# Optimization experiments

Measured on AMD Instinct MI355X. Metric: run time of the kernel, lower is better.

Reference implementation:

```python
import jax, jax.numpy as jnp
import numpy as np

N_NODES = 100000
N_EDGES = 1600000
IN, HID, OUT = 64, 64, 32


def setup_inputs() -> dict:
    key = jax.random.key(0)
    ks = jax.random.split(key, 8)
    x = jax.random.normal(ks[0], (N_NODES, IN), dtype=jnp.float32)
    src = jax.random.randint(ks[1], (N_EDGES,), 0, N_NODES)
    dst = jax.random.randint(ks[2], (N_EDGES,), 0, N_NODES)
    s = 0.05
    return {
        "x": x,
        "src": src,
        "dst": dst,
        "W_self1": jax.random.normal(ks[3], (IN, HID), dtype=jnp.float32) * s,
        "W_neigh1": jax.random.normal(ks[4], (IN, HID), dtype=jnp.float32) * s,
        "b1": jnp.zeros((HID,), dtype=jnp.float32),
        "W_self2": jax.random.normal(ks[5], (HID, OUT), dtype=jnp.float32) * s,
        "W_neigh2": jax.random.normal(ks[6], (HID, OUT), dtype=jnp.float32) * s,
        "b2": jnp.zeros((OUT,), dtype=jnp.float32),
    }


def reference(x, src, dst, W_self1, W_neigh1, b1, W_self2, W_neigh2, b2):
    n = x.shape[0]
    # in-degree per destination node; mean reducer yields 0 for isolated nodes
    deg = jax.ops.segment_sum(jnp.ones_like(dst, dtype=x.dtype), dst, num_segments=n)
    denom = jnp.maximum(deg, 1.0)[:, None]  # [N, 1]

    def sage_conv(h, W_self, W_neigh, b):
        # gather src features, sum into dst, divide by in-degree -> mean aggregation
        agg = jax.ops.segment_sum(h[src], dst, num_segments=n) / denom  # [N, F]
        return h @ W_self + agg @ W_neigh + b

    h = jax.nn.relu(sage_conv(x, W_self1, W_neigh1, b1))
    return sage_conv(h, W_self2, W_neigh2, b2)
```

## Files before the change

### kernel.cpp

```cpp
#include <hip/hip_runtime.h>

#define NF 64
#define OF 32

#define NPB 512
#define NPB_SHIFT 9
#define BCAP 12288
#define BIN_CHUNK 4096

typedef unsigned int uint;
typedef unsigned short ushort;
typedef __attribute__((ext_vector_type(8))) short bf16x8;
typedef __attribute__((ext_vector_type(4))) float f32x4;


__device__ __forceinline__ ushort f2bf(float f) {
    uint u = __float_as_uint(f);
    uint r = (u + 0x7fffu + ((u >> 16) & 1u)) >> 16;
    return (ushort)r;
}
__device__ __forceinline__ float bf2f(ushort b) { return __uint_as_float(((uint)b) << 16); }
__device__ __forceinline__ float blo(uint u) { return __uint_as_float(u << 16); }
__device__ __forceinline__ float bhi(uint u) { return __uint_as_float(u & 0xffff0000u); }


__global__ __launch_bounds__(256) void binning_kernel(
        const int* __restrict__ src, const int* __restrict__ dst, int n_edges,
        int* __restrict__ gcur, uint* __restrict__ stage) {
    __shared__ int hist[256];
    __shared__ int lofs[256];
    __shared__ int gbase[256];
    __shared__ int lrank[256];
    __shared__ uint lsorted[BIN_CHUNK];
    __shared__ unsigned char lbkt[BIN_CHUNK];

    int t = threadIdx.x;
    hist[t] = 0;
    lrank[t] = 0;
    __syncthreads();

    int e0 = blockIdx.x * BIN_CHUNK;
    int base_e = e0 + t * 16;
    int nloc = min(16, max(0, n_edges - base_e));

    uint es[16], ed[16];
    if (nloc == 16) {
#pragma unroll
        for (int q = 0; q < 4; q++) {
            uint4 s4 = *(const uint4*)(src + base_e + q * 4);
            uint4 d4 = *(const uint4*)(dst + base_e + q * 4);
            es[q * 4 + 0] = s4.x; es[q * 4 + 1] = s4.y; es[q * 4 + 2] = s4.z; es[q * 4 + 3] = s4.w;
            ed[q * 4 + 0] = d4.x; ed[q * 4 + 1] = d4.y; ed[q * 4 + 2] = d4.z; ed[q * 4 + 3] = d4.w;
        }
    } else {
        for (int j = 0; j < nloc; j++) {
            es[j] = (uint)src[base_e + j];
            ed[j] = (uint)dst[base_e + j];
        }
    }

    for (int j = 0; j < nloc; j++)
        atomicAdd(&hist[ed[j] >> NPB_SHIFT], 1);
    __syncthreads();

    int hv = hist[t];
    lofs[t] = hv;
    __syncthreads();
    for (int off = 1; off < 256; off <<= 1) {
        int u = (t >= off) ? lofs[t - off] : 0;
        __syncthreads();
        lofs[t] += u;
        __syncthreads();
    }
    int incl = lofs[t];
    __syncthreads();
    lofs[t] = incl - hv;
    if (hv > 0) gbase[t] = atomicAdd(&gcur[t], hv);
    __syncthreads();

    for (int j = 0; j < nloc; j++) {
        int b = ed[j] >> NPB_SHIFT;
        int r = atomicAdd(&lrank[b], 1);
        int pos = lofs[b] + r;
        lsorted[pos] = ((ed[j] & (NPB - 1)) << 17) | es[j];
        lbkt[pos] = (unsigned char)b;
    }
    __syncthreads();

    int bcnt = min(BIN_CHUNK, n_edges - e0);
    for (int i = t; i < bcnt; i += 256) {
        int b = lbkt[i];
        int pos = gbase[b] + (i - lofs[b]);
        if (pos < BCAP) stage[(size_t)b * BCAP + pos] = lsorted[i];
    }
}

__global__ __launch_bounds__(256) void build_kernel(
        const uint* __restrict__ stage, const int* __restrict__ gcnt,
        int* __restrict__ row_ptr, int* __restrict__ csr, int n, int nb) {
    __shared__ int bsc[256];
    __shared__ int ncnt[NPB];
    __shared__ int lcur[NPB];
    __shared__ int psum[256];
    __shared__ int lcsr[BCAP];

    int b = blockIdx.x;
    int t = threadIdx.x;

    bsc[t] = (t < nb) ? gcnt[t] : 0;
    __syncthreads();
    for (int off = 1; off < 256; off <<= 1) {
        int u = (t >= off) ? bsc[t - off] : 0;
        __syncthreads();
        bsc[t] += u;
        __syncthreads();
    }
    int gbase = (b == 0) ? 0 : bsc[b - 1];

    int cnt = min(gcnt[b], BCAP);
    int node0 = b << NPB_SHIFT;
    const uint* st = stage + (size_t)b * BCAP;

    ncnt[t] = 0;
    ncnt[t + 256] = 0;
    __syncthreads();
    for (int i = t; i < cnt; i += 256)
        atomicAdd(&ncnt[st[i] >> 17], 1);
    __syncthreads();

    int a0 = ncnt[2 * t], a1 = ncnt[2 * t + 1];
    psum[t] = a0 + a1;
    __syncthreads();
    for (int off = 1; off < 256; off <<= 1) {
        int u = (t >= off) ? psum[t - off] : 0;
        __syncthreads();
        psum[t] += u;
        __syncthreads();
    }
    int excl = (t == 0) ? 0 : psum[t - 1];
    int off0 = excl, off1 = excl + a0;
    int g0 = node0 + 2 * t, g1 = node0 + 2 * t + 1;
    if (g0 < n) row_ptr[g0] = gbase + off0;
    if (g1 < n) row_ptr[g1] = gbase + off1;
    lcur[2 * t] = off0;
    lcur[2 * t + 1] = off1;
    __syncthreads();

    for (int i = t; i < cnt; i += 256) {
        uint p = st[i];
        int slot = atomicAdd(&lcur[p >> 17], 1);
        lcsr[slot] = (int)(p & 0x1FFFFu);
    }
    __syncthreads();
    for (int i = t; i < cnt; i += 256)
        csr[gbase + i] = lcsr[i];

    if (b == nb - 1 && t == 0) row_ptr[n] = bsc[nb - 1];
}


__global__ void convert_prep_kernel(const float* __restrict__ in, ushort* __restrict__ out, int n4,
                                    const float* __restrict__ Ws1, const float* __restrict__ Wn1,
                                    const float* __restrict__ Ws2, const float* __restrict__ Wn2,
                                    ushort* __restrict__ wt1, ushort* __restrict__ wt2,
                                    int* __restrict__ gcur) {
    int i = blockIdx.x * blockDim.x + threadIdx.x;
    if (blockIdx.x == 0) gcur[threadIdx.x] = 0;
    if (i < n4) {
        float4 v = *(const float4*)(in + (size_t)i * 4);
        ushort4 o;
        o.x = f2bf(v.x); o.y = f2bf(v.y); o.z = f2bf(v.z); o.w = f2bf(v.w);
        *(ushort4*)(out + (size_t)i * 4) = o;
    }
    if (i < NF * 128) {
        int c = i >> 7, k = i & 127;
        float v = (k < 64) ? Ws1[k * NF + c] : Wn1[(k - 64) * NF + c];
        wt1[i] = f2bf(v);
    }
    if (i < OF * 128) {
        int c = i >> 7, k = i & 127;
        float v = (k < 64) ? Ws2[k * OF + c] : Wn2[(k - 64) * OF + c];
        wt2[i] = f2bf(v);
    }
}


template<int FW>
__global__ __launch_bounds__(256) void gather_kernel(
        const ushort* __restrict__ feat,
        const int* __restrict__ row_ptr, const int* __restrict__ csr,
        ushort* __restrict__ agg, int n) {
    constexpr int LPG = FW / 8;
    constexpr int NPW = 64 / LPG;
    int lane = threadIdx.x & 63;
    int g = lane / LPG;
    int fo = (lane % LPG) * 8;
    int wave = blockIdx.x * 4 + (threadIdx.x >> 6);
    int stride = gridDim.x * 4 * NPW;

    for (int n0 = wave * NPW + g; n0 < n; n0 += stride) {
        int beg = row_ptr[n0], end = row_ptr[n0 + 1];
        int cnt = end - beg;
        int full = beg + (cnt & ~7);
        float a0 = 0.f, a1 = 0.f, a2 = 0.f, a3 = 0.f;
        float a4 = 0.f, a5 = 0.f, a6 = 0.f, a7 = 0.f;
        for (int o = beg; o < full; o += 8) {
            uint4 v[8];
#pragma unroll
            for (int j = 0; j < 8; j++)
                v[j] = *(const uint4*)(feat + (size_t)csr[o + j] * FW + fo);
#pragma unroll
            for (int j = 0; j < 8; j++) {
                a0 += blo(v[j].x); a1 += bhi(v[j].x);
                a2 += blo(v[j].y); a3 += bhi(v[j].y);
                a4 += blo(v[j].z); a5 += bhi(v[j].z);
                a6 += blo(v[j].w); a7 += bhi(v[j].w);
            }
        }
        if (full < end) {
            uint4 v[8];
#pragma unroll
            for (int j = 0; j < 8; j++) {
                int e = min(full + j, end - 1);
                v[j] = *(const uint4*)(feat + (size_t)csr[e] * FW + fo);
            }
#pragma unroll
            for (int j = 0; j < 8; j++) {
                bool ok = (full + j) < end;
                uint vx = ok ? v[j].x : 0u, vy = ok ? v[j].y : 0u;
                uint vz = ok ? v[j].z : 0u, vw = ok ? v[j].w : 0u;
                a0 += blo(vx); a1 += bhi(vx);
                a2 += blo(vy); a3 += bhi(vy);
                a4 += blo(vz); a5 += bhi(vz);
                a6 += blo(vw); a7 += bhi(vw);
            }
        }
        float inv = 1.0f / (float)max(cnt, 1);
        uint4 o4;
        o4.x = (uint)f2bf(a0 * inv) | ((uint)f2bf(a1 * inv) << 16);
        o4.y = (uint)f2bf(a2 * inv) | ((uint)f2bf(a3 * inv) << 16);
        o4.z = (uint)f2bf(a4 * inv) | ((uint)f2bf(a5 * inv) << 16);
        o4.w = (uint)f2bf(a6 * inv) | ((uint)f2bf(a7 * inv) << 16);
        *(uint4*)(agg + (size_t)n0 * FW + fo) = o4;
    }
}


__global__ __launch_bounds__(256) void gemm1_fused_kernel(
        const ushort* __restrict__ xb, const ushort* __restrict__ aggx,
        const ushort* __restrict__ wt1,
        const ushort* __restrict__ wt2,
        const float* __restrict__ b1,
        ushort* __restrict__ hb, ushort* __restrict__ un2, int n, int ntiles) {
    __shared__ char tiles[4][2048];
    int lane = threadIdx.x & 63;
    int wslot = threadIdx.x >> 6;
    char* tile = tiles[wslot];
    int col = lane & 15, kg = lane >> 4;
    int wid = blockIdx.x * 4 + wslot;
    int nw = gridDim.x * 4;
    int sw = (col & 7) << 4;

    bf16x8 wfrag[4][4];
#pragma unroll
    for (int ct = 0; ct < 4; ct++)
#pragma unroll
        for (int kt = 0; kt < 4; kt++)
            wfrag[ct][kt] = *(const bf16x8*)(wt1 + ((ct * 16 + col) * 128 + kt * 32 + kg * 8));
    bf16x8 wn2frag[2][2];
#pragma unroll
    for (int c2 = 0; c2 < 2; c2++)
#pragma unroll
        for (int kt = 0; kt < 2; kt++)
            wn2frag[c2][kt] = *(const bf16x8*)(wt2 + ((c2 * 16 + col) * 128 + 64 + kt * 32 + kg * 8));
    float4 bias4[4];
#pragma unroll
    for (int ct = 0; ct < 4; ct++) bias4[ct] = *(const float4*)(b1 + ct * 16 + kg * 4);

    for (int t = wid; t < ntiles; t += nw) {
        int r0 = t * 16;
        int row = min(r0 + col, n - 1);
        const ushort* xrow = xb + (size_t)row * NF;
        const ushort* arow = aggx + (size_t)row * NF;
        bf16x8 nfrag[4];
        nfrag[0] = *(const bf16x8*)(xrow + kg * 8);
        nfrag[1] = *(const bf16x8*)(xrow + 32 + kg * 8);
        nfrag[2] = *(const bf16x8*)(arow + kg * 8);
        nfrag[3] = *(const bf16x8*)(arow + 32 + kg * 8);

        int node = r0 + col;
        bool ok = node < n;
#pragma unroll
        for (int ct = 0; ct < 4; ct++) {
            f32x4 c = {0.f, 0.f, 0.f, 0.f};
#pragma unroll
            for (int kt = 0; kt < 4; kt++)
                c = __builtin_amdgcn_mfma_f32_16x16x32_bf16(wfrag[ct][kt], nfrag[kt], c, 0, 0, 0);
            uint2 pk;
            pk.x = (uint)f2bf(fmaxf(c[0] + bias4[ct].x, 0.f))
                 | ((uint)f2bf(fmaxf(c[1] + bias4[ct].y, 0.f)) << 16);
            pk.y = (uint)f2bf(fmaxf(c[2] + bias4[ct].z, 0.f))
                 | ((uint)f2bf(fmaxf(c[3] + bias4[ct].w, 0.f)) << 16);
            *(uint2*)(tile + col * 128 + ((ct * 32 + kg * 8) ^ sw)) = pk;
            if (ok) *(uint2*)(hb + (size_t)node * NF + ct * 16 + kg * 4) = pk;
        }

        bf16x8 hfrag[2];
        hfrag[0] = *(const bf16x8*)(tile + col * 128 + ((0 * 64 + kg * 16) ^ sw));
        hfrag[1] = *(const bf16x8*)(tile + col * 128 + ((1 * 64 + kg * 16) ^ sw));
#pragma unroll
        for (int c2 = 0; c2 < 2; c2++) {
            f32x4 c = {0.f, 0.f, 0.f, 0.f};
            c = __builtin_amdgcn_mfma_f32_16x16x32_bf16(wn2frag[c2][0], hfrag[0], c, 0, 0, 0);
            c = __builtin_amdgcn_mfma_f32_16x16x32_bf16(wn2frag[c2][1], hfrag[1], c, 0, 0, 0);
            if (ok) {
                uint2 pk;
                pk.x = (uint)f2bf(c[0]) | ((uint)f2bf(c[1]) << 16);
                pk.y = (uint)f2bf(c[2]) | ((uint)f2bf(c[3]) << 16);
                *(uint2*)(un2 + (size_t)node * OF + c2 * 16 + kg * 4) = pk;
            }
        }
    }
}


__global__ __launch_bounds__(256) void gemm2_kernel(
        const ushort* __restrict__ hb, const ushort* __restrict__ aggu,
        const ushort* __restrict__ wt2,
        const float* __restrict__ b2,
        float* __restrict__ out, int n, int ntiles) {
    int lane = threadIdx.x & 63;
    int col = lane & 15, kg = lane >> 4;
    int wid = blockIdx.x * 4 + (threadIdx.x >> 6);
    int nw = gridDim.x * 4;

    bf16x8 wfrag[2][2];
#pragma unroll
    for (int ct = 0; ct < 2; ct++)
#pragma unroll
        for (int kt = 0; kt < 2; kt++)
            wfrag[ct][kt] = *(const bf16x8*)(wt2 + ((ct * 16 + col) * 128 + kt * 32 + kg * 8));
    float4 bias4[2];
#pragma unroll
    for (int ct = 0; ct < 2; ct++) bias4[ct] = *(const float4*)(b2 + ct * 16 + kg * 4);

    for (int t = wid; t < ntiles; t += nw) {
        int r0 = t * 16;
        int row = min(r0 + col, n - 1);
        const ushort* hrow = hb + (size_t)row * NF;
        bf16x8 nfrag[2];
        nfrag[0] = *(const bf16x8*)(hrow + kg * 8);
        nfrag[1] = *(const bf16x8*)(hrow + 32 + kg * 8);

        int node = r0 + col;
        bool ok = node < n;
#pragma unroll
        for (int ct = 0; ct < 2; ct++) {
            f32x4 c = {0.f, 0.f, 0.f, 0.f};
            c = __builtin_amdgcn_mfma_f32_16x16x32_bf16(wfrag[ct][0], nfrag[0], c, 0, 0, 0);
            c = __builtin_amdgcn_mfma_f32_16x16x32_bf16(wfrag[ct][1], nfrag[1], c, 0, 0, 0);
            if (ok) {
                uint2 au = *(const uint2*)(aggu + (size_t)node * OF + ct * 16 + kg * 4);
                float4 o;
                o.x = c[0] + bias4[ct].x + blo(au.x);
                o.y = c[1] + bias4[ct].y + bhi(au.x);
                o.z = c[2] + bias4[ct].z + blo(au.y);
                o.w = c[3] + bias4[ct].w + bhi(au.y);
                *(float4*)(out + (size_t)node * OF + ct * 16 + kg * 4) = o;
            }
        }
    }
}


extern "C" void kernel_launch(void* const* d_in, const int* in_sizes, int n_in,
                              void* d_out, int out_size, void* d_ws, size_t ws_size,
                              hipStream_t stream) {
    const float* x   = (const float*)d_in[0];
    const int*   src = (const int*)d_in[1];
    const int*   dst = (const int*)d_in[2];
    const float* Ws1 = (const float*)d_in[3];
    const float* Wn1 = (const float*)d_in[4];
    const float* b1  = (const float*)d_in[5];
    const float* Ws2 = (const float*)d_in[6];
    const float* Wn2 = (const float*)d_in[7];
    const float* b2  = (const float*)d_in[8];
    float* out = (float*)d_out;

    int n_nodes = in_sizes[0] / NF;
    int n_edges = in_sizes[1];
    int nb = (n_nodes + NPB - 1) >> NPB_SHIFT;

    auto align4k = [](size_t v) { return (v + 4095) & ~(size_t)4095; };
    char* ws = (char*)d_ws;
    size_t gcur_b = align4k(256 * 4);
    size_t rp_b   = align4k(((size_t)n_nodes + 1) * 4);
    size_t csr_b  = align4k((size_t)n_edges * 4);
    size_t xb_b   = align4k((size_t)n_nodes * NF * 2);
    size_t hb_b   = xb_b;
    size_t agg_b  = xb_b;
    size_t un2_b  = align4k((size_t)n_nodes * OF * 2);
    int* gcur        = (int*)ws;
    int* row_ptr     = (int*)(ws + gcur_b);
    int* csr         = (int*)(ws + gcur_b + rp_b);
    ushort* xb       = (ushort*)(ws + gcur_b + rp_b + csr_b);
    ushort* hb       = (ushort*)(ws + gcur_b + rp_b + csr_b + xb_b);
    ushort* agg      = (ushort*)(ws + gcur_b + rp_b + csr_b + xb_b + hb_b);
    uint*   stage    = (uint*)agg;
    ushort* aggu     = agg;
    ushort* un2      = (ushort*)(ws + gcur_b + rp_b + csr_b + xb_b + hb_b + agg_b);
    ushort* wt1      = (ushort*)(ws + gcur_b + rp_b + csr_b + xb_b + hb_b + agg_b + un2_b);
    ushort* wt2      = wt1 + NF * 128;

    int bin_blocks = (n_edges + BIN_CHUNK - 1) / BIN_CHUNK;
    int n4      = n_nodes * NF / 4;
    int cblocks = (n4 + 255) / 256;
    int ntiles  = (n_nodes + 15) / 16;
    int mblocks = 512;

    convert_prep_kernel<<<cblocks, 256, 0, stream>>>(x, xb, n4, Ws1, Wn1, Ws2, Wn2, wt1, wt2, gcur);
    binning_kernel<<<bin_blocks, 256, 0, stream>>>(src, dst, n_edges, gcur, stage);
    build_kernel<<<nb, 256, 0, stream>>>(stage, gcur, row_ptr, csr, n_nodes, nb);

    gather_kernel<64><<<2048, 256, 0, stream>>>(xb, row_ptr, csr, agg, n_nodes);
    gemm1_fused_kernel<<<mblocks, 256, 0, stream>>>(xb, agg, wt1, wt2, b1, hb, un2, n_nodes, ntiles);

    gather_kernel<32><<<1024, 256, 0, stream>>>(un2, row_ptr, csr, aggu, n_nodes);
    gemm2_kernel<<<mblocks, 256, 0, stream>>>(hb, aggu, wt2, b2, out, n_nodes, ntiles);
}
```

Baseline: 115.5 us.

## Fuse x conversion into binning launch, widen CSR build, unroll gather by 16

```diff
diff --git a/kernel.cpp b/kernel.cpp
--- a/kernel.cpp
+++ b/kernel.cpp
@@ -24,7 +24,27 @@
 __device__ __forceinline__ float bhi(uint u) { return __uint_as_float(u & 0xffff0000u); }
 
 
-__global__ __launch_bounds__(256) void binning_kernel(
+__global__ void zw_kernel(const float* __restrict__ Ws1, const float* __restrict__ Wn1,
+                          const float* __restrict__ Ws2, const float* __restrict__ Wn2,
+                          ushort* __restrict__ wt1, ushort* __restrict__ wt2,
+                          int* __restrict__ gcur) {
+    int i = blockIdx.x * blockDim.x + threadIdx.x;
+    if (blockIdx.x == 0) gcur[threadIdx.x] = 0;
+    if (i < NF * 128) {
+        int c = i >> 7, k = i & 127;
+        float v = (k < 64) ? Ws1[k * NF + c] : Wn1[(k - 64) * NF + c];
+        wt1[i] = f2bf(v);
+    }
+    if (i < OF * 128) {
+        int c = i >> 7, k = i & 127;
+        float v = (k < 64) ? Ws2[k * OF + c] : Wn2[(k - 64) * OF + c];
+        wt2[i] = f2bf(v);
+    }
+}
+
+
+__global__ __launch_bounds__(256) void convbin_kernel(
+        const float* __restrict__ x, ushort* __restrict__ xb, int n4, int cblocks,
         const int* __restrict__ src, const int* __restrict__ dst, int n_edges,
         int* __restrict__ gcur, uint* __restrict__ stage) {
     __shared__ int hist[256];
@@ -34,12 +54,23 @@
     __shared__ uint lsorted[BIN_CHUNK];
     __shared__ unsigned char lbkt[BIN_CHUNK];
 
+    if ((int)blockIdx.x < cblocks) {
+        int i = blockIdx.x * 256 + threadIdx.x;
+        if (i < n4) {
+            float4 v = *(const float4*)(x + (size_t)i * 4);
+            ushort4 o;
+            o.x = f2bf(v.x); o.y = f2bf(v.y); o.z = f2bf(v.z); o.w = f2bf(v.w);
+            *(ushort4*)(xb + (size_t)i * 4) = o;
+        }
+        return;
+    }
+
     int t = threadIdx.x;
     hist[t] = 0;
     lrank[t] = 0;
     __syncthreads();
 
-    int e0 = blockIdx.x * BIN_CHUNK;
+    int e0 = ((int)blockIdx.x - cblocks) * BIN_CHUNK;
     int base_e = e0 + t * 16;
     int nloc = min(16, max(0, n_edges - base_e));
 
@@ -95,24 +126,25 @@
     }
 }
 
-__global__ __launch_bounds__(256) void build_kernel(
+
+__global__ __launch_bounds__(512) void build_kernel(
         const uint* __restrict__ stage, const int* __restrict__ gcnt,
         int* __restrict__ row_ptr, int* __restrict__ csr, int n, int nb) {
     __shared__ int bsc[256];
     __shared__ int ncnt[NPB];
     __shared__ int lcur[NPB];
-    __shared__ int psum[256];
+    __shared__ int psum[512];
     __shared__ int lcsr[BCAP];
 
     int b = blockIdx.x;
     int t = threadIdx.x;
 
-    bsc[t] = (t < nb) ? gcnt[t] : 0;
+    if (t < 256) bsc[t] = (t < nb) ? gcnt[t] : 0;
     __syncthreads();
     for (int off = 1; off < 256; off <<= 1) {
-        int u = (t >= off) ? bsc[t - off] : 0;
-        __syncthreads();
-        bsc[t] += u;
+        int u = (t >= off && t < 256) ? bsc[t - off] : 0;
+        __syncthreads();
+        if (t < 256) bsc[t] += u;
         __syncthreads();
     }
     int gbase = (b == 0) ? 0 : bsc[b - 1];
@@ -122,66 +154,36 @@
     const uint* st = stage + (size_t)b * BCAP;
 
     ncnt[t] = 0;
-    ncnt[t + 256] = 0;
-    __syncthreads();
-    for (int i = t; i < cnt; i += 256)
+    __syncthreads();
+    for (int i = t; i < cnt; i += 512)
         atomicAdd(&ncnt[st[i] >> 17], 1);
     __syncthreads();
 
-    int a0 = ncnt[2 * t], a1 = ncnt[2 * t + 1];
-    psum[t] = a0 + a1;
-    __syncthreads();
-    for (int off = 1; off < 256; off <<= 1) {
+    int v = ncnt[t];
+    psum[t] = v;
+    __syncthreads();
+    for (int off = 1; off < 512; off <<= 1) {
         int u = (t >= off) ? psum[t - off] : 0;
         __syncthreads();
         psum[t] += u;
         __syncthreads();
     }
-    int excl = (t == 0) ? 0 : psum[t - 1];
-    int off0 = excl, off1 = excl + a0;
-    int g0 = node0 + 2 * t, g1 = node0 + 2 * t + 1;
-    if (g0 < n) row_ptr[g0] = gbase + off0;
-    if (g1 < n) row_ptr[g1] = gbase + off1;
-    lcur[2 * t] = off0;
-    lcur[2 * t + 1] = off1;
-    __syncthreads();
-
-    for (int i = t; i < cnt; i += 256) {
+    int excl = psum[t] - v;
+    int g0 = node0 + t;
+    if (g0 < n) row_ptr[g0] = gbase + excl;
+    lcur[t] = excl;
+    __syncthreads();
+
+    for (int i = t; i < cnt; i += 512) {
         uint p = st[i];
         int slot = atomicAdd(&lcur[p >> 17], 1);
         lcsr[slot] = (int)(p & 0x1FFFFu);
     }
     __syncthreads();
-    for (int i = t; i < cnt; i += 256)
+    for (int i = t; i < cnt; i += 512)
         csr[gbase + i] = lcsr[i];
 
     if (b == nb - 1 && t == 0) row_ptr[n] = bsc[nb - 1];
-}
-
-
-__global__ void convert_prep_kernel(const float* __restrict__ in, ushort* __restrict__ out, int n4,
-                                    const float* __restrict__ Ws1, const float* __restrict__ Wn1,
-                                    const float* __restrict__ Ws2, const float* __restrict__ Wn2,
-                                    ushort* __restrict__ wt1, ushort* __restrict__ wt2,
-                                    int* __restrict__ gcur) {
-    int i = blockIdx.x * blockDim.x + threadIdx.x;
-    if (blockIdx.x == 0) gcur[threadIdx.x] = 0;
-    if (i < n4) {
-        float4 v = *(const float4*)(in + (size_t)i * 4);
-        ushort4 o;
-        o.x = f2bf(v.x); o.y = f2bf(v.y); o.z = f2bf(v.z); o.w = f2bf(v.w);
-        *(ushort4*)(out + (size_t)i * 4) = o;
-    }
-    if (i < NF * 128) {
-        int c = i >> 7, k = i & 127;
-        float v = (k < 64) ? Ws1[k * NF + c] : Wn1[(k - 64) * NF + c];
-        wt1[i] = f2bf(v);
-    }
-    if (i < OF * 128) {
-        int c = i >> 7, k = i & 127;
-        float v = (k < 64) ? Ws2[k * OF + c] : Wn2[(k - 64) * OF + c];
-        wt2[i] = f2bf(v);
-    }
 }
 
 
@@ -201,16 +203,16 @@
     for (int n0 = wave * NPW + g; n0 < n; n0 += stride) {
         int beg = row_ptr[n0], end = row_ptr[n0 + 1];
         int cnt = end - beg;
-        int full = beg + (cnt & ~7);
+        int full = beg + (cnt & ~15);
         float a0 = 0.f, a1 = 0.f, a2 = 0.f, a3 = 0.f;
         float a4 = 0.f, a5 = 0.f, a6 = 0.f, a7 = 0.f;
-        for (int o = beg; o < full; o += 8) {
-            uint4 v[8];
-#pragma unroll
-            for (int j = 0; j < 8; j++)
+        for (int o = beg; o < full; o += 16) {
+            uint4 v[16];
+#pragma unroll
+            for (int j = 0; j < 16; j++)
                 v[j] = *(const uint4*)(feat + (size_t)csr[o + j] * FW + fo);
 #pragma unroll
-            for (int j = 0; j < 8; j++) {
+            for (int j = 0; j < 16; j++) {
                 a0 += blo(v[j].x); a1 += bhi(v[j].x);
                 a2 += blo(v[j].y); a3 += bhi(v[j].y);
                 a4 += blo(v[j].z); a5 += bhi(v[j].z);
@@ -218,14 +220,14 @@
             }
         }
         if (full < end) {
-            uint4 v[8];
-#pragma unroll
-            for (int j = 0; j < 8; j++) {
+            uint4 v[16];
+#pragma unroll
+            for (int j = 0; j < 16; j++) {
                 int e = min(full + j, end - 1);
                 v[j] = *(const uint4*)(feat + (size_t)csr[e] * FW + fo);
             }
 #pragma unroll
-            for (int j = 0; j < 8; j++) {
+            for (int j = 0; j < 16; j++) {
                 bool ok = (full + j) < end;
                 uint vx = ok ? v[j].x : 0u, vy = ok ? v[j].y : 0u;
                 uint vz = ok ? v[j].z : 0u, vw = ok ? v[j].w : 0u;
@@ -418,9 +420,10 @@
     int ntiles  = (n_nodes + 15) / 16;
     int mblocks = 512;
 
-    convert_prep_kernel<<<cblocks, 256, 0, stream>>>(x, xb, n4, Ws1, Wn1, Ws2, Wn2, wt1, wt2, gcur);
-    binning_kernel<<<bin_blocks, 256, 0, stream>>>(src, dst, n_edges, gcur, stage);
-    build_kernel<<<nb, 256, 0, stream>>>(stage, gcur, row_ptr, csr, n_nodes, nb);
+    zw_kernel<<<(NF * 128 + 255) / 256, 256, 0, stream>>>(Ws1, Wn1, Ws2, Wn2, wt1, wt2, gcur);
+    convbin_kernel<<<cblocks + bin_blocks, 256, 0, stream>>>(x, xb, n4, cblocks,
+                                                             src, dst, n_edges, gcur, stage);
+    build_kernel<<<nb, 512, 0, stream>>>(stage, gcur, row_ptr, csr, n_nodes, nb);
 
     gather_kernel<64><<<2048, 256, 0, stream>>>(xb, row_ptr, csr, agg, n_nodes);
     gemm1_fused_kernel<<<mblocks, 256, 0, stream>>>(xb, agg, wt1, wt2, b1, hb, un2, n_nodes, ntiles);
```

Result: slower. 118.3 us (+2.4%).

## Fuse layer-2 self GEMM into layer-1 kernel and accumulate neighbor mean into output

Applied to the files above, without the earlier changes.

```diff
diff --git a/kernel.cpp b/kernel.cpp
--- a/kernel.cpp
+++ b/kernel.cpp
@@ -185,12 +185,11 @@
 }
 
 
-template<int FW>
 __global__ __launch_bounds__(256) void gather_kernel(
         const ushort* __restrict__ feat,
         const int* __restrict__ row_ptr, const int* __restrict__ csr,
         ushort* __restrict__ agg, int n) {
-    constexpr int LPG = FW / 8;
+    constexpr int LPG = NF / 8;
     constexpr int NPW = 64 / LPG;
     int lane = threadIdx.x & 63;
     int g = lane / LPG;
@@ -208,7 +207,7 @@
             uint4 v[8];
 #pragma unroll
             for (int j = 0; j < 8; j++)
-                v[j] = *(const uint4*)(feat + (size_t)csr[o + j] * FW + fo);
+                v[j] = *(const uint4*)(feat + (size_t)csr[o + j] * NF + fo);
 #pragma unroll
             for (int j = 0; j < 8; j++) {
                 a0 += blo(v[j].x); a1 += bhi(v[j].x);
@@ -222,7 +221,7 @@
 #pragma unroll
             for (int j = 0; j < 8; j++) {
                 int e = min(full + j, end - 1);
-                v[j] = *(const uint4*)(feat + (size_t)csr[e] * FW + fo);
+                v[j] = *(const uint4*)(feat + (size_t)csr[e] * NF + fo);
             }
 #pragma unroll
             for (int j = 0; j < 8; j++) {
@@ -241,7 +240,68 @@
         o4.y = (uint)f2bf(a2 * inv) | ((uint)f2bf(a3 * inv) << 16);
         o4.z = (uint)f2bf(a4 * inv) | ((uint)f2bf(a5 * inv) << 16);
         o4.w = (uint)f2bf(a6 * inv) | ((uint)f2bf(a7 * inv) << 16);
-        *(uint4*)(agg + (size_t)n0 * FW + fo) = o4;
+        *(uint4*)(agg + (size_t)n0 * NF + fo) = o4;
+    }
+}
+
+
+__global__ __launch_bounds__(256) void gather_acc_kernel(
+        const ushort* __restrict__ un2,
+        const int* __restrict__ row_ptr, const int* __restrict__ csr,
+        float* __restrict__ out, int n) {
+    constexpr int LPG = OF / 8;
+    constexpr int NPW = 64 / LPG;
+    int lane = threadIdx.x & 63;
+    int g = lane / LPG;
+    int fo = (lane % LPG) * 8;
+    int wave = blockIdx.x * 4 + (threadIdx.x >> 6);
+    int stride = gridDim.x * 4 * NPW;
+
+    for (int n0 = wave * NPW + g; n0 < n; n0 += stride) {
+        int beg = row_ptr[n0], end = row_ptr[n0 + 1];
+        int cnt = end - beg;
+        int full = beg + (cnt & ~7);
+        float a0 = 0.f, a1 = 0.f, a2 = 0.f, a3 = 0.f;
+        float a4 = 0.f, a5 = 0.f, a6 = 0.f, a7 = 0.f;
+        for (int o = beg; o < full; o += 8) {
+            uint4 v[8];
+#pragma unroll
+            for (int j = 0; j < 8; j++)
+                v[j] = *(const uint4*)(un2 + (size_t)csr[o + j] * OF + fo);
+#pragma unroll
+            for (int j = 0; j < 8; j++) {
+                a0 += blo(v[j].x); a1 += bhi(v[j].x);
+                a2 += blo(v[j].y); a3 += bhi(v[j].y);
+                a4 += blo(v[j].z); a5 += bhi(v[j].z);
+                a6 += blo(v[j].w); a7 += bhi(v[j].w);
+            }
+        }
+        if (full < end) {
+            uint4 v[8];
+#pragma unroll
+            for (int j = 0; j < 8; j++) {
+                int e = min(full + j, end - 1);
+                v[j] = *(const uint4*)(un2 + (size_t)csr[e] * OF + fo);
+            }
+#pragma unroll
+            for (int j = 0; j < 8; j++) {
+                bool ok = (full + j) < end;
+                uint vx = ok ? v[j].x : 0u, vy = ok ? v[j].y : 0u;
+                uint vz = ok ? v[j].z : 0u, vw = ok ? v[j].w : 0u;
+                a0 += blo(vx); a1 += bhi(vx);
+                a2 += blo(vy); a3 += bhi(vy);
+                a4 += blo(vz); a5 += bhi(vz);
+                a6 += blo(vw); a7 += bhi(vw);
+            }
+        }
+        float inv = 1.0f / (float)max(cnt, 1);
+        float* op = out + (size_t)n0 * OF + fo;
+        float4 o0 = *(const float4*)op;
+        float4 o1 = *(const float4*)(op + 4);
+        o0.x += a0 * inv; o0.y += a1 * inv; o0.z += a2 * inv; o0.w += a3 * inv;
+        o1.x += a4 * inv; o1.y += a5 * inv; o1.z += a6 * inv; o1.w += a7 * inv;
+        *(float4*)op = o0;
+        *(float4*)(op + 4) = o1;
     }
 }
 
@@ -251,7 +311,9 @@
         const ushort* __restrict__ wt1,
         const ushort* __restrict__ wt2,
         const float* __restrict__ b1,
-        ushort* __restrict__ hb, ushort* __restrict__ un2, int n, int ntiles) {
+        const float* __restrict__ b2,
+        ushort* __restrict__ hb, ushort* __restrict__ un2,
+        float* __restrict__ out, int n, int ntiles) {
     __shared__ char tiles[4][2048];
     int lane = threadIdx.x & 63;
     int wslot = threadIdx.x >> 6;
@@ -268,14 +330,20 @@
         for (int kt = 0; kt < 4; kt++)
             wfrag[ct][kt] = *(const bf16x8*)(wt1 + ((ct * 16 + col) * 128 + kt * 32 + kg * 8));
     bf16x8 wn2frag[2][2];
+    bf16x8 ws2frag[2][2];
 #pragma unroll
     for (int c2 = 0; c2 < 2; c2++)
 #pragma unroll
-        for (int kt = 0; kt < 2; kt++)
+        for (int kt = 0; kt < 2; kt++) {
             wn2frag[c2][kt] = *(const bf16x8*)(wt2 + ((c2 * 16 + col) * 128 + 64 + kt * 32 + kg * 8));
+            ws2frag[c2][kt] = *(const bf16x8*)(wt2 + ((c2 * 16 + col) * 128 + kt * 32 + kg * 8));
+        }
     float4 bias4[4];
 #pragma unroll
     for (int ct = 0; ct < 4; ct++) bias4[ct] = *(const float4*)(b1 + ct * 16 + kg * 4);
+    float4 bias2_4[2];
+#pragma unroll
+    for (int c2 = 0; c2 < 2; c2++) bias2_4[c2] = *(const float4*)(b2 + c2 * 16 + kg * 4);
 
     for (int t = wid; t < ntiles; t += nw) {
         int r0 = t * 16;
@@ -313,60 +381,20 @@
             f32x4 c = {0.f, 0.f, 0.f, 0.f};
             c = __builtin_amdgcn_mfma_f32_16x16x32_bf16(wn2frag[c2][0], hfrag[0], c, 0, 0, 0);
             c = __builtin_amdgcn_mfma_f32_16x16x32_bf16(wn2frag[c2][1], hfrag[1], c, 0, 0, 0);
+            f32x4 s = {0.f, 0.f, 0.f, 0.f};
+            s = __builtin_amdgcn_mfma_f32_16x16x32_bf16(ws2frag[c2][0], hfrag[0], s, 0, 0, 0);
+            s = __builtin_amdgcn_mfma_f32_16x16x32_bf16(ws2frag[c2][1], hfrag[1], s, 0, 0, 0);
             if (ok) {
                 uint2 pk;
                 pk.x = (uint)f2bf(c[0]) | ((uint)f2bf(c[1]) << 16);
                 pk.y = (uint)f2bf(c[2]) | ((uint)f2bf(c[3]) << 16);
                 *(uint2*)(un2 + (size_t)node * OF + c2 * 16 + kg * 4) = pk;
-            }
-        }
-    }
-}
-
-
-__global__ __launch_bounds__(256) void gemm2_kernel(
-        const ushort* __restrict__ hb, const ushort* __restrict__ aggu,
-        const ushort* __restrict__ wt2,
-        const float* __restrict__ b2,
-        float* __restrict__ out, int n, int ntiles) {
-    int lane = threadIdx.x & 63;
-    int col = lane & 15, kg = lane >> 4;
-    int wid = blockIdx.x * 4 + (threadIdx.x >> 6);
-    int nw = gridDim.x * 4;
-
-    bf16x8 wfrag[2][2];
-#pragma unroll
-    for (int ct = 0; ct < 2; ct++)
-#pragma unroll
-        for (int kt = 0; kt < 2; kt++)
-            wfrag[ct][kt] = *(const bf16x8*)(wt2 + ((ct * 16 + col) * 128 + kt * 32 + kg * 8));
-    float4 bias4[2];
-#pragma unroll
-    for (int ct = 0; ct < 2; ct++) bias4[ct] = *(const float4*)(b2 + ct * 16 + kg * 4);
-
-    for (int t = wid; t < ntiles; t += nw) {
-        int r0 = t * 16;
-        int row = min(r0 + col, n - 1);
-        const ushort* hrow = hb + (size_t)row * NF;
-        bf16x8 nfrag[2];
-        nfrag[0] = *(const bf16x8*)(hrow + kg * 8);
-        nfrag[1] = *(const bf16x8*)(hrow + 32 + kg * 8);
-
-        int node = r0 + col;
-        bool ok = node < n;
-#pragma unroll
-        for (int ct = 0; ct < 2; ct++) {
-            f32x4 c = {0.f, 0.f, 0.f, 0.f};
-            c = __builtin_amdgcn_mfma_f32_16x16x32_bf16(wfrag[ct][0], nfrag[0], c, 0, 0, 0);
-            c = __builtin_amdgcn_mfma_f32_16x16x32_bf16(wfrag[ct][1], nfrag[1], c, 0, 0, 0);
-            if (ok) {
-                uint2 au = *(const uint2*)(aggu + (size_t)node * OF + ct * 16 + kg * 4);
                 float4 o;
-                o.x = c[0] + bias4[ct].x + blo(au.x);
-                o.y = c[1] + bias4[ct].y + bhi(au.x);
-                o.z = c[2] + bias4[ct].z + blo(au.y);
-                o.w = c[3] + bias4[ct].w + bhi(au.y);
-                *(float4*)(out + (size_t)node * OF + ct * 16 + kg * 4) = o;
+                o.x = s[0] + bias2_4[c2].x;
+                o.y = s[1] + bias2_4[c2].y;
+                o.z = s[2] + bias2_4[c2].z;
+                o.w = s[3] + bias2_4[c2].w;
+                *(float4*)(out + (size_t)node * OF + c2 * 16 + kg * 4) = o;
             }
         }
     }
@@ -407,7 +435,6 @@
     ushort* hb       = (ushort*)(ws + gcur_b + rp_b + csr_b + xb_b);
     ushort* agg      = (ushort*)(ws + gcur_b + rp_b + csr_b + xb_b + hb_b);
     uint*   stage    = (uint*)agg;
-    ushort* aggu     = agg;
     ushort* un2      = (ushort*)(ws + gcur_b + rp_b + csr_b + xb_b + hb_b + agg_b);
     ushort* wt1      = (ushort*)(ws + gcur_b + rp_b + csr_b + xb_b + hb_b + agg_b + un2_b);
     ushort* wt2      = wt1 + NF * 128;
@@ -422,9 +449,9 @@
     binning_kernel<<<bin_blocks, 256, 0, stream>>>(src, dst, n_edges, gcur, stage);
     build_kernel<<<nb, 256, 0, stream>>>(stage, gcur, row_ptr, csr, n_nodes, nb);
 
-    gather_kernel<64><<<2048, 256, 0, stream>>>(xb, row_ptr, csr, agg, n_nodes);
-    gemm1_fused_kernel<<<mblocks, 256, 0, stream>>>(xb, agg, wt1, wt2, b1, hb, un2, n_nodes, ntiles);
-
-    gather_kernel<32><<<1024, 256, 0, stream>>>(un2, row_ptr, csr, aggu, n_nodes);
-    gemm2_kernel<<<mblocks, 256, 0, stream>>>(hb, aggu, wt2, b2, out, n_nodes, ntiles);
-}
+    gather_kernel<<<2048, 256, 0, stream>>>(xb, row_ptr, csr, agg, n_nodes);
+    gemm1_fused_kernel<<<mblocks, 256, 0, stream>>>(xb, agg, wt1, wt2, b1, b2,
+                                                    hb, un2, out, n_nodes, ntiles);
+
+    gather_acc_kernel<<<1024, 256, 0, stream>>>(un2, row_ptr, csr, out, n_nodes);
+}
```

Result: no change. 113.8 us (median of 2 runs) (-1.5%).
